# Performance work log

Measured on AMD Instinct MI355X. Metric: run time of the kernel, lower is better.

The kernel has to match this reference:

```python
import jax, jax.numpy as jnp
import numpy as np

VA, HA = 8, 8
N_NODES = 2 * VA * HA  # 128 graph nodes (rgb + ir anchor tokens)
N_LAYERS = 8
EPS = 1e-5


def setup_inputs() -> dict:
    key = jax.random.key(0)
    ks = jax.random.split(key, 6)
    B, C, H, W = 64, 512, 32, 32
    E = 1024
    rgb_fea = jax.random.normal(ks[0], (B, C, H, W), jnp.float32)
    ir_fea = jax.random.normal(ks[1], (B, C, H, W), jnp.float32)
    edge_index = jax.random.randint(ks[2], (2, E), 0, N_NODES, dtype=jnp.int64)
    pos_emb = jax.random.normal(ks[3], (1, N_NODES, C), jnp.float32) * 0.02
    W_gcn = jax.random.normal(ks[4], (N_LAYERS, C, C), jnp.float32) * 0.02  # [in,out] per layer
    b_gcn = jnp.zeros((N_LAYERS, C), jnp.float32)
    ln_w = jnp.ones((C,), jnp.float32)
    ln_b = jnp.zeros((C,), jnp.float32)
    return dict(rgb_fea=rgb_fea, ir_fea=ir_fea, edge_index=edge_index,
                pos_emb=pos_emb, W_gcn=W_gcn, b_gcn=b_gcn, ln_w=ln_w, ln_b=ln_b)


def _adaptive_avgpool(x, va, ha):
    # exact for H%va==0, W%ha==0 (32 -> 8): mean over 4x4 blocks
    B, C, H, W = x.shape
    return x.reshape(B, C, va, H // va, ha, W // ha).mean(axis=(3, 5))


def _gcn_norm(edge_index, n):
    # PyG gcn_norm with self loops: deg over target, norm = d^-1/2[src]*d^-1/2[dst]
    loop = jnp.arange(n, dtype=edge_index.dtype)
    src = jnp.concatenate([edge_index[0], loop])
    dst = jnp.concatenate([edge_index[1], loop])
    deg = jnp.zeros((n,), jnp.float32).at[dst].add(1.0)
    dinv = jnp.where(deg > 0, jax.lax.rsqrt(deg), 0.0)
    return src, dst, dinv[src] * dinv[dst]


def _gcn_layer(x, W, b, src, dst, norm):
    # x: [B,N,C] -> linear, gather from src, weight, scatter-add to dst, + bias
    xw = jnp.einsum('bnd,de->bne', x, W)
    msg = xw[:, src, :] * norm[None, :, None]  # [B,E,C]
    agg = jnp.zeros_like(xw).at[:, dst, :].add(msg)
    return agg + b


def reference(rgb_fea, ir_fea, edge_index, pos_emb, W_gcn, b_gcn, ln_w, ln_b):
    B, C = rgb_fea.shape[0], rgb_fea.shape[1]
    r = _adaptive_avgpool(rgb_fea, VA, HA).reshape(B, C, -1)  # [B,C,64]
    i = _adaptive_avgpool(ir_fea, VA, HA).reshape(B, C, -1)   # [B,C,64]
    tok = jnp.concatenate([r, i], axis=2).transpose(0, 2, 1)  # [B,128,C]
    x = pos_emb + tok  # dropout is identity in eval
    src, dst, norm = _gcn_norm(edge_index, N_NODES)
    for l in range(W_gcn.shape[0]):
        x = jax.nn.relu(_gcn_layer(x, W_gcn[l], b_gcn[l], src, dst, norm))
    mu = x.mean(-1, keepdims=True)
    var = x.var(-1, keepdims=True)
    x = (x - mu) * jax.lax.rsqrt(var + EPS) * ln_w + ln_b
    x = x.reshape(B, 2, VA, HA, C).transpose(0, 1, 4, 2, 3)  # [B,2,C,8,8]
    rgb_out = x[:, 0]
    ir_out = x[:, 1]
    return rgb_out, ir_out
```

## Files before the change

### kernel.cpp

```cpp
#include <hip/hip_runtime.h>

#define B_      64
#define C_      512
#define NNODE   128
#define NEDGE   1024
#define NLAYERS 8
#define EPS_    1e-5f

typedef __attribute__((ext_vector_type(8))) short bf16x8;
typedef __attribute__((ext_vector_type(4))) float f32x4;
typedef const __attribute__((address_space(1))) unsigned int* gas_p;
typedef __attribute__((address_space(3))) unsigned int* las_p;

__device__ __forceinline__ ushort f2b(float x) {
    unsigned u = __builtin_bit_cast(unsigned, x);
    unsigned r = (u + 0x7fffu + ((u >> 16) & 1u)) >> 16;
    return (ushort)r;
}
__device__ __forceinline__ float b2f(ushort h) {
    unsigned u = ((unsigned)h) << 16;
    return __builtin_bit_cast(float, u);
}


__global__ __launch_bounds__(256) void prep_k(const int* __restrict__ ei,
                                              ushort* __restrict__ Ah,
                                              ushort* __restrict__ Al) {
    __shared__ float A_L[NNODE * NNODE];
    __shared__ int degI[NNODE];
    __shared__ float dinvL[NNODE];
    const int t = threadIdx.x;

    if (t < NNODE) degI[t] = 0;
    for (int i = t; i < NNODE * NNODE / 4; i += 256)
        *(f32x4*)&A_L[i * 4] = (f32x4){0.f, 0.f, 0.f, 0.f};
    __syncthreads();
    for (int e = t; e < NEDGE; e += 256) atomicAdd(&degI[ei[NEDGE + e]], 1);
    __syncthreads();
    if (t < NNODE) dinvL[t] = rsqrtf((float)degI[t] + 1.0f);
    __syncthreads();
    for (int e = t; e < NEDGE; e += 256) {
        int s = ei[e], d = ei[NEDGE + e];
        atomicAdd(&A_L[d * NNODE + s], dinvL[s] * dinvL[d]);
    }
    if (t < NNODE) atomicAdd(&A_L[t * NNODE + t], dinvL[t] * dinvL[t]);
    __syncthreads();
    for (int i = 0; i < 8; ++i) {
        int gid = i * 256 + t;
        int lane = gid & 63, lr = lane & 15, lq = lane >> 4;
        int kk = (gid >> 6) & 3, mf = (gid >> 8) & 3, wm = (gid >> 10) & 1;
        int row = wm * 64 + mf * 16 + lr;
        int k = kk * 32 + lq * 8;
        ushort hh[8], ll[8];
#pragma unroll
        for (int j = 0; j < 8; ++j) {
            float v = A_L[row * NNODE + k + j];
            hh[j] = f2b(v);
            ll[j] = f2b(v - b2f(hh[j]));
        }
        *(int4*)&Ah[(size_t)gid * 8] = *(int4*)hh;
        *(int4*)&Al[(size_t)gid * 8] = *(int4*)ll;
    }
}

__global__ __launch_bounds__(256) void front_k(const float* __restrict__ rgb,
                                               const float* __restrict__ ir,
                                               const float* __restrict__ pos,
                                               const float* __restrict__ W,
                                               ushort* __restrict__ xh,
                                               ushort* __restrict__ xl,
                                               ushort* __restrict__ Wfh,
                                               ushort* __restrict__ Wfl) {
    __shared__ __align__(16) char lbuf[17408];
    const int t = threadIdx.x;
    const int bid = blockIdx.x;

    if (bid < 2048) {
        float (*lds)[130] = (float(*)[130])lbuf;
        const int l = t & 63, wv = t >> 6;
        const int c0 = (bid & 31) * 16, b = bid >> 5;
        const int va = l >> 3, ha = l & 7;

        for (int i = 0; i < 8; i += 2) {
            f32x4 r[2][4];
#pragma unroll
            for (int j = 0; j < 2; ++j) {
                int p = wv * 8 + i + j;
                int src = p >> 4, cc = p & 15;
                const float* base = (src ? ir : rgb)
                    + ((size_t)(b * C_ + c0 + cc)) * 1024 + va * 128 + ha * 4;
#pragma unroll
                for (int r2 = 0; r2 < 4; ++r2)
                    r[j][r2] = __builtin_nontemporal_load((const f32x4*)(base + r2 * 32));
            }
#pragma unroll
            for (int j = 0; j < 2; ++j) {
                int p = wv * 8 + i + j;
                int src = p >> 4, cc = p & 15;
                float s = 0.f;
#pragma unroll
                for (int r2 = 0; r2 < 4; ++r2)
                    s += r[j][r2].x + r[j][r2].y + r[j][r2].z + r[j][r2].w;
                lds[cc][src * 64 + l] = s * 0.0625f;
            }
        }
        __syncthreads();

        const int n = t >> 1, cb = (t & 1) * 8;
        float v[8];
        {
            float4 p0 = *(const float4*)&pos[(size_t)n * C_ + c0 + cb];
            float4 p1 = *(const float4*)&pos[(size_t)n * C_ + c0 + cb + 4];
            v[0] = lds[cb + 0][n] + p0.x; v[1] = lds[cb + 1][n] + p0.y;
            v[2] = lds[cb + 2][n] + p0.z; v[3] = lds[cb + 3][n] + p0.w;
            v[4] = lds[cb + 4][n] + p1.x; v[5] = lds[cb + 5][n] + p1.y;
            v[6] = lds[cb + 6][n] + p1.z; v[7] = lds[cb + 7][n] + p1.w;
        }
        ushort hs[8], ls[8];
#pragma unroll
        for (int j = 0; j < 8; ++j) {
            hs[j] = f2b(v[j]);
            ls[j] = f2b(v[j] - b2f(hs[j]));
        }
        const int wm = n >> 6, mf = (n >> 4) & 3, lr = n & 15;
        const int c = c0 + cb;
        const int ks = c >> 5, lq = (c >> 3) & 3;
        size_t o = (((size_t)(b * 2 + wm) * 4 + mf) * 16 + ks) * 512 + (lq * 16 + lr) * 8;
        *(int4*)&xh[o] = *(int4*)&hs[0];
        *(int4*)&xl[o] = *(int4*)&ls[0];
    } else {
        float (*tl)[68] = (float(*)[68])lbuf;
        const int wid = bid - 2048;
        const int n0 = (wid & 7) * 64, k0 = ((wid >> 3) & 7) * 64, l = wid >> 6;
        const float* Wl = W + (size_t)l * C_ * C_;
        {
            int kk = t >> 2, nc = (t & 3) * 16;
            const float* src = Wl + (size_t)(k0 + kk) * C_ + n0 + nc;
#pragma unroll
            for (int g = 0; g < 4; ++g)
                *(float4*)&tl[kk][nc + g * 4] = *(const float4*)(src + g * 4);
        }
        __syncthreads();
        {
            int nn = t >> 2, kc = (t & 3) * 16;
            int n = n0 + nn;
            int nb = n >> 4, lr = n & 15;
            ushort h[16], lo[16];
#pragma unroll
            for (int j = 0; j < 16; ++j) {
                float v = tl[kc + j][nn];
                h[j] = f2b(v);
                lo[j] = f2b(v - b2f(h[j]));
            }
#pragma unroll
            for (int g = 0; g < 2; ++g) {
                int kb = k0 + kc + g * 8;
                int ks = kb >> 5, lq = (kb >> 3) & 3;
                size_t o = (((size_t)l * 32 + nb) * 16 + ks) * 512 + (lq * 16 + lr) * 8;
                *(int4*)&Wfh[o] = *(int4*)&h[g * 8];
                *(int4*)&Wfl[o] = *(int4*)&lo[g * 8];
            }
        }
    }
}

__global__ __launch_bounds__(512, 2) void gemm_fused_k(
    const ushort* __restrict__ Xfh, const ushort* __restrict__ Xfl,
    const ushort* __restrict__ Wfh, const ushort* __restrict__ Wfl,
    const ushort* __restrict__ Afh, const ushort* __restrict__ Afl,
    const float* __restrict__ bias,
    ushort* __restrict__ Yfh, ushort* __restrict__ Yfl) {
    __shared__ __align__(16) char smem[65536];
    ushort* sPh = (ushort*)smem;
    ushort* sPl = (ushort*)(smem + 32768);
    float*  sT  = (float*)smem;

    const int t = threadIdx.x, lane = t & 63;
    const int wv = t >> 6, wm = wv >> 2, wn = wv & 3;
    const int lr = lane & 15, lq = lane >> 4;
    const int bid = blockIdx.x;
    const int xcd = bid & 7, slot = bid >> 3;
    const int b = xcd * 8 + (slot >> 2);
    const int nt = slot & 3;
    const int bn = nt * 128;

    const ushort* srcXh = Xfh + (size_t)b * 65536 + (size_t)wv * 8192 + lane * 8;
    const ushort* srcXl = Xfl + (size_t)b * 65536 + (size_t)wv * 8192 + lane * 8;
    const ushort* srcWh = Wfh + (size_t)(nt * 8 + wv) * 8192 + lane * 8;
    const ushort* srcWl = Wfl + (size_t)(nt * 8 + wv) * 8192 + lane * 8;

#define STAGE(KS, BUF)                                                        \
    {                                                                         \
        char* dstb = smem + (BUF) * 32768;                                    \
        __builtin_amdgcn_global_load_lds((gas_p)(srcXh + (KS) * 512),         \
            (las_p)(dstb + wv * 1024), 16, 0, 0);                             \
        __builtin_amdgcn_global_load_lds((gas_p)(srcXl + (KS) * 512),         \
            (las_p)(dstb + (8 + wv) * 1024), 16, 0, 0);                       \
        __builtin_amdgcn_global_load_lds((gas_p)(srcWh + (KS) * 512),         \
            (las_p)(dstb + (16 + wv) * 1024), 16, 0, 0);                      \
        __builtin_amdgcn_global_load_lds((gas_p)(srcWl + (KS) * 512),         \
            (las_p)(dstb + (24 + wv) * 1024), 16, 0, 0);                      \
    }

    f32x4 acc[4][2];
#pragma unroll
    for (int i = 0; i < 4; ++i)
#pragma unroll
        for (int j = 0; j < 2; ++j) acc[i][j] = (f32x4){0.f, 0.f, 0.f, 0.f};

    float bv[2];
#pragma unroll
    for (int nf = 0; nf < 2; ++nf) bv[nf] = bias[bn + wn * 32 + nf * 16 + lr];

    STAGE(0, 0)
    int cur = 0;
    for (int ks = 0; ks < 16; ++ks) {
        __syncthreads();
        if (ks < 15) STAGE(ks + 1, cur ^ 1)
        const char* sb = smem + cur * 32768;
        bf16x8 fah[4], fal[4], fbh[2], fbl[2];
#pragma unroll
        for (int mf = 0; mf < 4; ++mf) {
            fah[mf] = *(const bf16x8*)(sb + (wm * 4 + mf) * 1024 + lane * 16);
            fal[mf] = *(const bf16x8*)(sb + (8 + wm * 4 + mf) * 1024 + lane * 16);
        }
#pragma unroll
        for (int nf = 0; nf < 2; ++nf) {
            fbh[nf] = *(const bf16x8*)(sb + (16 + wn * 2 + nf) * 1024 + lane * 16);
            fbl[nf] = *(const bf16x8*)(sb + (24 + wn * 2 + nf) * 1024 + lane * 16);
        }
#pragma unroll
        for (int mf = 0; mf < 4; ++mf)
#pragma unroll
            for (int nf = 0; nf < 2; ++nf) {
                acc[mf][nf] = __builtin_amdgcn_mfma_f32_16x16x32_bf16(
                    fah[mf], fbh[nf], acc[mf][nf], 0, 0, 0);
                acc[mf][nf] = __builtin_amdgcn_mfma_f32_16x16x32_bf16(
                    fal[mf], fbh[nf], acc[mf][nf], 0, 0, 0);
                acc[mf][nf] = __builtin_amdgcn_mfma_f32_16x16x32_bf16(
                    fah[mf], fbl[nf], acc[mf][nf], 0, 0, 0);
            }
        cur ^= 1;
    }
#undef STAGE
    __syncthreads();

#pragma unroll
    for (int mf = 0; mf < 4; ++mf) {
        int gm = wm * 8 + mf * 2 + (lq >> 1);
        int moff = (lq & 1) * 4;
#pragma unroll
        for (int nf = 0; nf < 2; ++nf) {
            int n = wn * 32 + nf * 16 + lr;
            int addr = n * 128 + ((gm ^ (n & 15)) << 3) + moff;
            ushort4 hu, lu;
            float y0 = acc[mf][nf][0], y1 = acc[mf][nf][1];
            float y2 = acc[mf][nf][2], y3 = acc[mf][nf][3];
            hu.x = f2b(y0); lu.x = f2b(y0 - b2f(hu.x));
            hu.y = f2b(y1); lu.y = f2b(y1 - b2f(hu.y));
            hu.z = f2b(y2); lu.z = f2b(y2 - b2f(hu.z));
            hu.w = f2b(y3); lu.w = f2b(y3 - b2f(hu.w));
            *(ushort4*)&sPh[addr] = hu;
            *(ushort4*)&sPl[addr] = lu;
        }
    }
    __syncthreads();

    f32x4 acc2[4][2];
#pragma unroll
    for (int i = 0; i < 4; ++i)
#pragma unroll
        for (int j = 0; j < 2; ++j) acc2[i][j] = (f32x4){0.f, 0.f, 0.f, 0.f};

#pragma unroll
    for (int kk = 0; kk < 4; ++kk) {
        bf16x8 gah[4], gal[4], gbh[2], gbl[2];
#pragma unroll
        for (int mf = 0; mf < 4; ++mf) {
            size_t o = (size_t)((wm * 4 + mf) * 4 + kk) * 512 + lane * 8;
            gah[mf] = *(const bf16x8*)&Afh[o];
            gal[mf] = *(const bf16x8*)&Afl[o];
        }
#pragma unroll
        for (int nf = 0; nf < 2; ++nf) {
            int n = wn * 32 + nf * 16 + lr;
            int g = (((kk * 4 + lq) ^ (n & 15)) << 3);
            gbh[nf] = *(const bf16x8*)&sPh[n * 128 + g];
            gbl[nf] = *(const bf16x8*)&sPl[n * 128 + g];
        }
#pragma unroll
        for (int mf = 0; mf < 4; ++mf)
#pragma unroll
            for (int nf = 0; nf < 2; ++nf) {
                acc2[mf][nf] = __builtin_amdgcn_mfma_f32_16x16x32_bf16(
                    gah[mf], gbh[nf], acc2[mf][nf], 0, 0, 0);
                acc2[mf][nf] = __builtin_amdgcn_mfma_f32_16x16x32_bf16(
                    gal[mf], gbh[nf], acc2[mf][nf], 0, 0, 0);
                acc2[mf][nf] = __builtin_amdgcn_mfma_f32_16x16x32_bf16(
                    gah[mf], gbl[nf], acc2[mf][nf], 0, 0, 0);
            }
    }

#pragma unroll
    for (int h = 0; h < 2; ++h) {
        __syncthreads();
        if ((wn >> 1) == h) {
#pragma unroll
            for (int mf = 0; mf < 4; ++mf)
#pragma unroll
                for (int nf = 0; nf < 2; ++nf) {
                    int mb = wm * 64 + mf * 16 + lq * 4;
                    int nl = (wn & 1) * 32 + nf * 16 + lr;
#pragma unroll
                    for (int r = 0; r < 4; ++r) {
                        float y = fmaxf(acc2[mf][nf][r] + bv[nf], 0.0f);
                        sT[(mb + r) * 68 + nl] = y;
                    }
                }
        }
        __syncthreads();
        {
            const int m = t >> 2, seg = t & 3;
            const float* rp = &sT[m * 68 + seg * 16];
            ushort hs[16], ls[16];
#pragma unroll
            for (int j = 0; j < 16; ++j) {
                float y = rp[j];
                hs[j] = f2b(y);
                ls[j] = f2b(y - b2f(hs[j]));
            }
            const int wm2 = m >> 6, mf2 = (m >> 4) & 3, lr2 = m & 15;
#pragma unroll
            for (int g = 0; g < 2; ++g) {
                int n_g = bn + h * 64 + seg * 16 + g * 8;
                int ks2 = n_g >> 5, lq2 = (n_g >> 3) & 3;
                size_t o = (((size_t)(b * 2 + wm2) * 4 + mf2) * 16 + ks2) * 512
                         + (lq2 * 16 + lr2) * 8;
                *(int4*)&Yfh[o] = *(int4*)&hs[g * 8];
                *(int4*)&Yfl[o] = *(int4*)&ls[g * 8];
            }
        }
    }
}

__global__ __launch_bounds__(256) void ln_out_k(const ushort* __restrict__ xh,
                                                const ushort* __restrict__ xl,
                                                const float* __restrict__ lw,
                                                const float* __restrict__ lb,
                                                float* __restrict__ out) {
    __shared__ float tile[32][68];
    __shared__ float muA[64], invA[64];
    const int t = threadIdx.x, lane = t & 63, mf = t >> 6;
    const int lr = lane & 15, lq = lane >> 4;
    const int b = blockIdx.x & 63, wm = blockIdx.x >> 6;
    const size_t base = ((size_t)(b * 2 + wm) * 4 + mf) * 8192 + lane * 8;

    float s1 = 0.f, s2 = 0.f;
    for (int ks = 0; ks < 16; ++ks) {
        int4 hh = *(const int4*)&xh[base + ks * 512];
        int4 llv = *(const int4*)&xl[base + ks * 512];
        ushort* hp = (ushort*)&hh;
        ushort* lp = (ushort*)&llv;
#pragma unroll
        for (int j = 0; j < 8; ++j) {
            float v = b2f(hp[j]) + b2f(lp[j]);
            s1 += v;
            s2 += v * v;
        }
    }
    s1 += __shfl_xor(s1, 16); s2 += __shfl_xor(s2, 16);
    s1 += __shfl_xor(s1, 32); s2 += __shfl_xor(s2, 32);
    if (lq == 0) {
        float mu = s1 * (1.0f / C_);
        muA[mf * 16 + lr] = mu;
        invA[mf * 16 + lr] = rsqrtf(s2 * (1.0f / C_) - mu * mu + EPS_);
    }
    __syncthreads();

    const int p = mf * 16 + lr;
    const float mu = muA[p], inv = invA[p];
    const size_t ob = (size_t)wm * (B_ * C_ * 64) + (size_t)b * (C_ * 64);

    for (int ks = 0; ks < 16; ++ks) {
        {
            int4 hh = *(const int4*)&xh[base + ks * 512];
            int4 llv = *(const int4*)&xl[base + ks * 512];
            ushort* hp = (ushort*)&hh;
            ushort* lp = (ushort*)&llv;
            int c = ks * 32 + lq * 8;
            float4 w0 = *(const float4*)&lw[c];
            float4 w1 = *(const float4*)&lw[c + 4];
            float4 b0 = *(const float4*)&lb[c];
            float4 b1 = *(const float4*)&lb[c + 4];
            float wv_[8] = {w0.x, w0.y, w0.z, w0.w, w1.x, w1.y, w1.z, w1.w};
            float bb_[8] = {b0.x, b0.y, b0.z, b0.w, b1.x, b1.y, b1.z, b1.w};
#pragma unroll
            for (int j = 0; j < 8; ++j) {
                float v = b2f(hp[j]) + b2f(lp[j]);
                tile[lq * 8 + j][p] = (v - mu) * inv * wv_[j] + bb_[j];
            }
        }
        __syncthreads();
        {
            int ch = t >> 3, p0 = (t & 7) * 8;
            float4 v0 = *(const float4*)&tile[ch][p0];
            float4 v1 = *(const float4*)&tile[ch][p0 + 4];
            *(float4*)&out[ob + (size_t)(ks * 32 + ch) * 64 + p0] = v0;
            *(float4*)&out[ob + (size_t)(ks * 32 + ch) * 64 + p0 + 4] = v1;
        }
        __syncthreads();
    }
}


extern "C" void kernel_launch(void* const* d_in, const int* in_sizes, int n_in,
                              void* d_out, int out_size, void* d_ws, size_t ws_size,
                              hipStream_t stream) {
    const float* rgb = (const float*)d_in[0];
    const float* ir  = (const float*)d_in[1];
    const int*   ei  = (const int*)d_in[2];
    const float* pos = (const float*)d_in[3];
    const float* Wg  = (const float*)d_in[4];
    const float* bg  = (const float*)d_in[5];
    const float* lw  = (const float*)d_in[6];
    const float* lb  = (const float*)d_in[7];
    float* out = (float*)d_out;

    char* ws = (char*)d_ws;
    ushort* x0h  = (ushort*)(ws);
    ushort* x0l  = (ushort*)(ws + 8388608);
    ushort* x1h  = (ushort*)(ws + 16777216);
    ushort* x1l  = (ushort*)(ws + 25165824);
    ushort* Wfh  = (ushort*)(ws + 33554432);
    ushort* Wfl  = (ushort*)(ws + 37748736);
    ushort* Afh  = (ushort*)(ws + 42009088);
    ushort* Afl  = (ushort*)(ws + 42041856);

    prep_k<<<1, 256, 0, stream>>>(ei, Afh, Afl);

    front_k<<<2560, 256, 0, stream>>>(rgb, ir, pos, Wg, x0h, x0l, Wfh, Wfl);

    for (int l = 0; l < NLAYERS; ++l) {
        const ushort* inh = (l & 1) ? x1h : x0h;
        const ushort* inl = (l & 1) ? x1l : x0l;
        ushort* outh = (l & 1) ? x0h : x1h;
        ushort* outl = (l & 1) ? x0l : x1l;
        gemm_fused_k<<<256, 512, 0, stream>>>(
            inh, inl, Wfh + (size_t)l * C_ * C_, Wfl + (size_t)l * C_ * C_,
            Afh, Afl, bg + (size_t)l * C_, outh, outl);
    }

    ln_out_k<<<2 * B_, 256, 0, stream>>>(x0h, x0l, lw, lb, out);
}
```

Before: 248.5 us.

## Halve GEMM block N-tile to 64 and double grid to 512 blocks

Measured after the change: 215.0 us. 1.16x faster.

```diff
diff --git a/kernel.cpp b/kernel.cpp
--- a/kernel.cpp
+++ b/kernel.cpp
@@ -164,42 +164,48 @@
     }
 }
 
-__global__ __launch_bounds__(512, 2) void gemm_fused_k(
+__global__ __launch_bounds__(256, 2) void gemm_fused_k(
     const ushort* __restrict__ Xfh, const ushort* __restrict__ Xfl,
     const ushort* __restrict__ Wfh, const ushort* __restrict__ Wfl,
     const ushort* __restrict__ Afh, const ushort* __restrict__ Afl,
     const float* __restrict__ bias,
     ushort* __restrict__ Yfh, ushort* __restrict__ Yfl) {
-    __shared__ __align__(16) char smem[65536];
+    __shared__ __align__(16) char smem[49152];
     ushort* sPh = (ushort*)smem;
-    ushort* sPl = (ushort*)(smem + 32768);
+    ushort* sPl = (ushort*)(smem + 16384);
     float*  sT  = (float*)smem;
 
     const int t = threadIdx.x, lane = t & 63;
-    const int wv = t >> 6, wm = wv >> 2, wn = wv & 3;
+    const int wv = t >> 6, wm = wv >> 1, wn = wv & 1;
     const int lr = lane & 15, lq = lane >> 4;
     const int bid = blockIdx.x;
     const int xcd = bid & 7, slot = bid >> 3;
-    const int b = xcd * 8 + (slot >> 2);
-    const int nt = slot & 3;
-    const int bn = nt * 128;
-
-    const ushort* srcXh = Xfh + (size_t)b * 65536 + (size_t)wv * 8192 + lane * 8;
-    const ushort* srcXl = Xfl + (size_t)b * 65536 + (size_t)wv * 8192 + lane * 8;
-    const ushort* srcWh = Wfh + (size_t)(nt * 8 + wv) * 8192 + lane * 8;
-    const ushort* srcWl = Wfl + (size_t)(nt * 8 + wv) * 8192 + lane * 8;
+    const int b = xcd * 8 + (slot >> 3);
+    const int nt8 = slot & 7;
+    const int bn = nt8 * 64;
+
+    const ushort* srcX0h = Xfh + (size_t)b * 65536 + (size_t)(wv * 2) * 8192 + lane * 8;
+    const ushort* srcX1h = srcX0h + 8192;
+    const ushort* srcX0l = Xfl + (size_t)b * 65536 + (size_t)(wv * 2) * 8192 + lane * 8;
+    const ushort* srcX1l = srcX0l + 8192;
+    const ushort* srcWh  = Wfh + (size_t)(nt8 * 4 + wv) * 8192 + lane * 8;
+    const ushort* srcWl  = Wfl + (size_t)(nt8 * 4 + wv) * 8192 + lane * 8;
 
 #define STAGE(KS, BUF)                                                        \
     {                                                                         \
-        char* dstb = smem + (BUF) * 32768;                                    \
-        __builtin_amdgcn_global_load_lds((gas_p)(srcXh + (KS) * 512),         \
-            (las_p)(dstb + wv * 1024), 16, 0, 0);                             \
-        __builtin_amdgcn_global_load_lds((gas_p)(srcXl + (KS) * 512),         \
-            (las_p)(dstb + (8 + wv) * 1024), 16, 0, 0);                       \
+        char* dstb = smem + (BUF) * 24576;                                    \
+        __builtin_amdgcn_global_load_lds((gas_p)(srcX0h + (KS) * 512),        \
+            (las_p)(dstb + (wv * 2 + 0) * 1024), 16, 0, 0);                   \
+        __builtin_amdgcn_global_load_lds((gas_p)(srcX1h + (KS) * 512),        \
+            (las_p)(dstb + (wv * 2 + 1) * 1024), 16, 0, 0);                   \
+        __builtin_amdgcn_global_load_lds((gas_p)(srcX0l + (KS) * 512),        \
+            (las_p)(dstb + (8 + wv * 2 + 0) * 1024), 16, 0, 0);               \
+        __builtin_amdgcn_global_load_lds((gas_p)(srcX1l + (KS) * 512),        \
+            (las_p)(dstb + (8 + wv * 2 + 1) * 1024), 16, 0, 0);               \
         __builtin_amdgcn_global_load_lds((gas_p)(srcWh + (KS) * 512),         \
             (las_p)(dstb + (16 + wv) * 1024), 16, 0, 0);                      \
         __builtin_amdgcn_global_load_lds((gas_p)(srcWl + (KS) * 512),         \
-            (las_p)(dstb + (24 + wv) * 1024), 16, 0, 0);                      \
+            (las_p)(dstb + (20 + wv) * 1024), 16, 0, 0);                      \
     }
 
     f32x4 acc[4][2];
@@ -217,7 +223,7 @@
     for (int ks = 0; ks < 16; ++ks) {
         __syncthreads();
         if (ks < 15) STAGE(ks + 1, cur ^ 1)
-        const char* sb = smem + cur * 32768;
+        const char* sb = smem + cur * 24576;
         bf16x8 fah[4], fal[4], fbh[2], fbl[2];
 #pragma unroll
         for (int mf = 0; mf < 4; ++mf) {
@@ -227,7 +233,7 @@
 #pragma unroll
         for (int nf = 0; nf < 2; ++nf) {
             fbh[nf] = *(const bf16x8*)(sb + (16 + wn * 2 + nf) * 1024 + lane * 16);
-            fbl[nf] = *(const bf16x8*)(sb + (24 + wn * 2 + nf) * 1024 + lane * 16);
+            fbl[nf] = *(const bf16x8*)(sb + (20 + wn * 2 + nf) * 1024 + lane * 16);
         }
 #pragma unroll
         for (int mf = 0; mf < 4; ++mf)
@@ -300,45 +306,42 @@
                     gah[mf], gbl[nf], acc2[mf][nf], 0, 0, 0);
             }
     }
-
-#pragma unroll
-    for (int h = 0; h < 2; ++h) {
-        __syncthreads();
-        if ((wn >> 1) == h) {
-#pragma unroll
-            for (int mf = 0; mf < 4; ++mf)
-#pragma unroll
-                for (int nf = 0; nf < 2; ++nf) {
-                    int mb = wm * 64 + mf * 16 + lq * 4;
-                    int nl = (wn & 1) * 32 + nf * 16 + lr;
-#pragma unroll
-                    for (int r = 0; r < 4; ++r) {
-                        float y = fmaxf(acc2[mf][nf][r] + bv[nf], 0.0f);
-                        sT[(mb + r) * 68 + nl] = y;
-                    }
-                }
-        }
-        __syncthreads();
-        {
-            const int m = t >> 2, seg = t & 3;
-            const float* rp = &sT[m * 68 + seg * 16];
-            ushort hs[16], ls[16];
-#pragma unroll
-            for (int j = 0; j < 16; ++j) {
-                float y = rp[j];
-                hs[j] = f2b(y);
-                ls[j] = f2b(y - b2f(hs[j]));
-            }
-            const int wm2 = m >> 6, mf2 = (m >> 4) & 3, lr2 = m & 15;
-#pragma unroll
-            for (int g = 0; g < 2; ++g) {
-                int n_g = bn + h * 64 + seg * 16 + g * 8;
-                int ks2 = n_g >> 5, lq2 = (n_g >> 3) & 3;
-                size_t o = (((size_t)(b * 2 + wm2) * 4 + mf2) * 16 + ks2) * 512
-                         + (lq2 * 16 + lr2) * 8;
-                *(int4*)&Yfh[o] = *(int4*)&hs[g * 8];
-                *(int4*)&Yfl[o] = *(int4*)&ls[g * 8];
-            }
+    __syncthreads();
+
+#pragma unroll
+    for (int mf = 0; mf < 4; ++mf) {
+#pragma unroll
+        for (int nf = 0; nf < 2; ++nf) {
+            int mb = wm * 64 + mf * 16 + lq * 4;
+            int nl = wn * 32 + nf * 16 + lr;
+#pragma unroll
+            for (int r = 0; r < 4; ++r) {
+                float y = fmaxf(acc2[mf][nf][r] + bv[nf], 0.0f);
+                sT[(mb + r) * 68 + nl] = y;
+            }
+        }
+    }
+    __syncthreads();
+
+    {
+        const int m = t >> 1, hw = t & 1;
+        const float* rp = &sT[m * 68 + hw * 32];
+        ushort hs[32], ls[32];
+#pragma unroll
+        for (int j = 0; j < 32; ++j) {
+            float y = rp[j];
+            hs[j] = f2b(y);
+            ls[j] = f2b(y - b2f(hs[j]));
+        }
+        const int wm2 = m >> 6, mf2 = (m >> 4) & 3, lr2 = m & 15;
+#pragma unroll
+        for (int g = 0; g < 4; ++g) {
+            int n_g = bn + hw * 32 + g * 8;
+            int ks2 = n_g >> 5, lq2 = (n_g >> 3) & 3;
+            size_t o = (((size_t)(b * 2 + wm2) * 4 + mf2) * 16 + ks2) * 512
+                     + (lq2 * 16 + lr2) * 8;
+            *(int4*)&Yfh[o] = *(int4*)&hs[g * 8];
+            *(int4*)&Yfl[o] = *(int4*)&ls[g * 8];
         }
     }
 }
@@ -445,7 +448,7 @@
         const ushort* inl = (l & 1) ? x1l : x0l;
         ushort* outh = (l & 1) ? x0h : x1h;
         ushort* outl = (l & 1) ? x0l : x1l;
-        gemm_fused_k<<<256, 512, 0, stream>>>(
+        gemm_fused_k<<<512, 256, 0, stream>>>(
             inh, inl, Wfh + (size_t)l * C_ * C_, Wfl + (size_t)l * C_ * C_,
             Afh, Afl, bg + (size_t)l * C_, outh, outl);
     }
```
